# Performance work log

Measured on AMD Instinct MI355X. Metric: run time of the kernel, lower is better.

Reference implementation:

```python
import jax, jax.numpy as jnp
import numpy as np

B, NSL, DS = 8, 12, 768
L, R, DL = 24, 64, 4096
DP = 4096
DIM_T = NSL * 2 * DS          # 18432
FUSED = 1024 + 512            # 1536
GEN_IN = FUSED + 256 + 64     # 1856


def setup_inputs() -> dict:
    key = jax.random.key(0)
    ks = jax.random.split(key, 16)
    s = lambda d: 1.0 / np.sqrt(d)
    return {
        "A_small": jax.random.normal(ks[0], (B, NSL, 1, DS), jnp.float32),
        "B_small": jax.random.normal(ks[1], (B, NSL, DS, 1), jnp.float32),
        "prompt_emb": jax.random.normal(ks[2], (B, DP), jnp.float32),
        "W_ct": jax.random.normal(ks[3], (DIM_T, 1024), jnp.float32) * s(DIM_T),
        "b_ct": jnp.zeros((1024,), jnp.float32),
        "W_cp": jax.random.normal(ks[4], (DP, 512), jnp.float32) * s(DP),
        "b_cp": jnp.zeros((512,), jnp.float32),
        "W_pc": jax.random.normal(ks[5], (FUSED, L), jnp.float32) * s(FUSED),
        "b_pc": jnp.zeros((L,), jnp.float32),
        "E_layer": jax.random.normal(ks[6], (L, 256), jnp.float32),
        "E_chunk": jax.random.normal(ks[7], (R, 64), jnp.float32),
        "W_A": jax.random.normal(ks[8], (GEN_IN, DL), jnp.float32) * s(GEN_IN),
        "b_A": jnp.zeros((DL,), jnp.float32),
        "W_B": jax.random.normal(ks[9], (GEN_IN, DL), jnp.float32) * s(GEN_IN),
        "b_B": jnp.zeros((DL,), jnp.float32),
    }


def reference(A_small, B_small, prompt_emb, W_ct, b_ct, W_cp, b_cp, W_pc, b_pc,
              E_layer, E_chunk, W_A, b_A, W_B, b_B):
    bsz = prompt_emb.shape[0]
    flat_T = jnp.concatenate([A_small.reshape(bsz, -1), B_small.reshape(bsz, -1)], axis=-1)
    t_feat = jax.nn.relu(flat_T @ W_ct + b_ct)          # [B,1024]
    p_feat = jax.nn.relu(prompt_emb @ W_cp + b_cp)      # [B,512]
    fused = jnp.concatenate([t_feat, p_feat], axis=-1)  # [B,1536]
    logits = fused @ W_pc + b_pc                        # [B,L]
    y_soft = jax.nn.sigmoid(logits)                     # eval mode (no gumbel)
    y_hard = (y_soft > 0.5).astype(y_soft.dtype)
    gate = y_soft + jax.lax.stop_gradient(y_hard - y_soft)  # straight-through

    # Batched hypernetwork over all (layer, chunk) pairs instead of a double loop.
    ctx = jnp.broadcast_to(fused[:, None, None, :], (bsz, L, R, FUSED))
    le = jnp.broadcast_to(E_layer[None, :, None, :], (bsz, L, R, 256))
    ce = jnp.broadcast_to(E_chunk[None, None, :, :], (bsz, L, R, 64))
    gen = jnp.concatenate([ctx, le, ce], axis=-1)       # [B,L,R,1856]

    A = gen @ W_A + b_A                                 # [B,L,R,DL]
    Bm = gen @ W_B + b_B                                # [B,L,R,DL]
    A_large = A * gate[:, :, None, None]                # [B,L,R,DL]
    B_large = jnp.transpose(Bm, (0, 1, 3, 2))           # [B,L,DL,R]
    return (A_large, B_large, gate)
```

## Files before the change

kernel.cpp:

```cpp
#include <hip/hip_runtime.h>

typedef float v4f __attribute__((ext_vector_type(4)));

#define NB 8
#define NL 24
#define NR 64
#define ND 4096
#define NFUSED 1536
#define NTF 1024
#define NPF 512
#define KP 4096

#define FKC 12

#define WS_FACC  0
#define WS_GATE  49152
#define WS_PLA   49344
#define WS_PLB   245952
#define WS_CA    442560
#define WS_CBT   704704
#define WS_PFA   966848
#define WS_PFB   1360064

__global__ __launch_bounds__(256) void k_indep(
    const float* __restrict__ As, const float* __restrict__ Bs,
    const float* __restrict__ W_ct,
    const float* __restrict__ prompt, const float* __restrict__ W_cp,
    const float* __restrict__ E_layer, const float* __restrict__ E_chunk,
    const float* __restrict__ W_A, const float* __restrict__ W_B,
    float* __restrict__ fAcc,
    float* __restrict__ pLA, float* __restrict__ pLB,
    float* __restrict__ CA, float* __restrict__ CBT) {
  __shared__ float e[NR * 64];
  const int bx = blockIdx.x;
  const int tid = threadIdx.x;

  if (bx < 576) {
    const int j = (bx & 3) * 256 + tid;
    const int kc = bx >> 2;
    const int kbase = kc * 128;
    float acc[NB] = {};
    for (int kk = 0; kk < 128; ++kk) {
      const int k = kbase + kk;
      const float w = W_ct[(size_t)k * NTF + j];
      const float* x = (k < 9216) ? (As + k) : (Bs + (k - 9216));
#pragma unroll
      for (int b = 0; b < NB; ++b) acc[b] = fmaf(x[b * 9216], w, acc[b]);
    }
    const int rep = kc & 3;
#pragma unroll
    for (int b = 0; b < NB; ++b)
      atomicAdd(fAcc + (size_t)(rep * NB + b) * NFUSED + j, acc[b]);
  } else if (bx < 640) {
    const int t = bx - 576;
    const int j = (t & 1) * 256 + tid;
    const int kc = t >> 1;
    const int kbase = kc * 128;
    float acc[NB] = {};
    for (int kk = 0; kk < 128; ++kk) {
      const int k = kbase + kk;
      const float w = W_cp[(size_t)k * NPF + j];
#pragma unroll
      for (int b = 0; b < NB; ++b) acc[b] = fmaf(prompt[b * KP + k], w, acc[b]);
    }
    const int rep = kc & 3;
#pragma unroll
    for (int b = 0; b < NB; ++b)
      atomicAdd(fAcc + (size_t)(rep * NB + b) * NFUSED + NTF + j, acc[b]);
  } else if (bx < 704) {
    const int t = bx - 640;
    const bool isA = t < 32;
    const int tt = isA ? t : t - 32;
    const int dc = tt & 15;
    const int kh = tt >> 4;
    const float* W = (isA ? W_A : W_B) + (size_t)(NFUSED + kh * 128) * ND;
    float* pL = (isA ? pLA : pLB) + (size_t)kh * NL * ND;
    const int d = dc * 256 + tid;
    float acc[NL] = {};
    for (int kk = 0; kk < 128; ++kk) {
      const float w = W[(size_t)kk * ND + d];
      const float* el = E_layer + kh * 128 + kk;
#pragma unroll
      for (int l = 0; l < NL; ++l) acc[l] = fmaf(el[l * 256], w, acc[l]);
    }
#pragma unroll
    for (int l = 0; l < NL; ++l) pL[(size_t)l * ND + d] = acc[l];
  } else {
    const int t = bx - 704;
    const bool isA = t < 16;
    const int tt = isA ? t : t - 16;
    const float* W = (isA ? W_A : W_B) + (size_t)(NFUSED + 256) * ND;
    for (int i = tid; i < NR * 64; i += 256) e[i] = E_chunk[i];
    __syncthreads();
    const int d = tt * 256 + tid;
    float w[64];
#pragma unroll
    for (int k = 0; k < 64; ++k) w[k] = W[(size_t)k * ND + d];
    for (int r = 0; r < NR; ++r) {
      float s = 0.f;
#pragma unroll
      for (int k = 0; k < 64; ++k) s = fmaf(e[r * 64 + k], w[k], s);
      if (isA) CA[(size_t)r * ND + d] = s;
      else     CBT[(size_t)d * NR + r] = s;
    }
  }
}

__global__ __launch_bounds__(256) void k_dep(
    const float* __restrict__ fAcc,
    const float* __restrict__ b_ct, const float* __restrict__ b_cp,
    const float* __restrict__ W_A, const float* __restrict__ W_B,
    const float* __restrict__ W_pc, const float* __restrict__ b_pc,
    float* __restrict__ pFA, float* __restrict__ pFB,
    float* __restrict__ gate_ws, float* __restrict__ gate_out) {
  __shared__ float sm[1664];
  const int bx = blockIdx.x;
  const int tid = threadIdx.x;

  if (bx < 384) {
    const bool isA = bx < 192;
    const int t = isA ? bx : bx - 192;
    const float* W = isA ? W_A : W_B;
    float* part = isA ? pFA : pFB;
    const int dc = t & 15;
    const int kc = t >> 4;
    const int kbase = kc * 128;

    for (int i = tid; i < 1024; i += 256) {
      const int b = i >> 7, kk = i & 127;
      const int k = kbase + kk;
      float v = (k < NTF) ? b_ct[k] : b_cp[k - NTF];
#pragma unroll
      for (int rep = 0; rep < 4; ++rep)
        v += fAcc[(size_t)(rep * NB + b) * NFUSED + k];
      sm[i] = fmaxf(v, 0.f);
    }
    __syncthreads();

    const int d = dc * 256 + tid;
    float acc[NB] = {};
    for (int kk = 0; kk < 128; ++kk) {
      const float w = W[(size_t)(kbase + kk) * ND + d];
#pragma unroll
      for (int b = 0; b < NB; ++b) acc[b] = fmaf(sm[b * 128 + kk], w, acc[b]);
    }
#pragma unroll
    for (int b = 0; b < NB; ++b)
      part[(size_t)(kc * NB + b) * ND + d] = acc[b];
  } else {
    const int b = bx - 384;
    for (int j = tid; j < NFUSED; j += 256) {
      float v = (j < NTF) ? b_ct[j] : b_cp[j - NTF];
#pragma unroll
      for (int rep = 0; rep < 4; ++rep)
        v += fAcc[(size_t)(rep * NB + b) * NFUSED + j];
      sm[j] = fmaxf(v, 0.f);
    }
    __syncthreads();
    float acc[NL] = {};
    for (int j = tid; j < NFUSED; j += 256) {
      const float f = sm[j];
#pragma unroll
      for (int l = 0; l < NL; ++l) acc[l] = fmaf(f, W_pc[j * NL + l], acc[l]);
    }
#pragma unroll
    for (int off = 32; off > 0; off >>= 1)
#pragma unroll
      for (int l = 0; l < NL; ++l) acc[l] += __shfl_down(acc[l], off);
    const int wave = tid >> 6, lane = tid & 63;
    if (lane == 0)
#pragma unroll
      for (int l = 0; l < NL; ++l) sm[NFUSED + wave * NL + l] = acc[l];
    __syncthreads();
    if (tid < NL) {
      float s = b_pc[tid];
#pragma unroll
      for (int w = 0; w < 4; ++w) s += sm[NFUSED + w * NL + tid];
      const float g = s > 0.f ? 1.f : 0.f;
      gate_ws[b * NL + tid] = g;
      gate_out[b * NL + tid] = g;
    }
  }
}

__global__ __launch_bounds__(256) void k_out(
    const float* __restrict__ pFA, const float* __restrict__ pFB,
    const float* __restrict__ b_A, const float* __restrict__ b_B,
    const float* __restrict__ pLA, const float* __restrict__ pLB,
    const float* __restrict__ CA, const float* __restrict__ CBT,
    const float* __restrict__ gate,
    float* __restrict__ outA, float* __restrict__ outB) {
  __shared__ float sbase[512];
  const int bx = blockIdx.x;
  const int tid = threadIdx.x;
  if (bx < 1536) {
    const int bl = bx >> 3;
    const int rest = bx & 7;
    const int b = bl / NL, l = bl % NL;
    const int d = (rest >> 1) * 1024 + tid * 4;
    const int r0 = (rest & 1) * 32;
    const float g = gate[bl];
    v4f base = *(const v4f*)(b_A + d);
#pragma unroll
    for (int kc = 0; kc < FKC; ++kc)
      base += *(const v4f*)(pFA + (size_t)(kc * NB + b) * ND + d);
    base += *(const v4f*)(pLA + (size_t)l * ND + d);
    base += *(const v4f*)(pLA + (size_t)(NL + l) * ND + d);
    float* outp = outA + ((size_t)bl * NR + r0) * ND + d;
#pragma unroll 4
    for (int r = 0; r < 32; ++r) {
      const v4f c = *(const v4f*)(CA + (size_t)(r0 + r) * ND + d);
      const v4f v = (base + c) * g;
      __builtin_nontemporal_store(v, (v4f*)outp);
      outp += ND;
    }
  } else {
    const int t = bx - 1536;
    const int bl = t >> 3;
    const int b = bl / NL, l = bl % NL;
    const int dbase = (t & 7) * 512;
    for (int dd = tid; dd < 512; dd += 256) {
      const int d = dbase + dd;
      float s = b_B[d] + pLB[(size_t)l * ND + d] + pLB[(size_t)(NL + l) * ND + d];
#pragma unroll
      for (int kc = 0; kc < FKC; ++kc)
        s += pFB[(size_t)(kc * NB + b) * ND + d];
      sbase[dd] = s;
    }
    __syncthreads();
    const int dd16 = tid >> 4;
    const int r4 = (tid & 15) * 4;
#pragma unroll 4
    for (int i = 0; i < 32; ++i) {
      const int dloc = i * 16 + dd16;
      const int d = dbase + dloc;
      const v4f c = *(const v4f*)(CBT + (size_t)d * NR + r4);
      const v4f v = c + sbase[dloc];
      __builtin_nontemporal_store(v, (v4f*)(outB + ((size_t)bl * ND + d) * NR + r4));
    }
  }
}

extern "C" void kernel_launch(void* const* d_in, const int* in_sizes, int n_in,
                              void* d_out, int out_size, void* d_ws, size_t ws_size,
                              hipStream_t stream) {
  const float* A_small   = (const float*)d_in[0];
  const float* B_small   = (const float*)d_in[1];
  const float* prompt    = (const float*)d_in[2];
  const float* W_ct      = (const float*)d_in[3];
  const float* b_ct      = (const float*)d_in[4];
  const float* W_cp      = (const float*)d_in[5];
  const float* b_cp      = (const float*)d_in[6];
  const float* W_pc      = (const float*)d_in[7];
  const float* b_pc      = (const float*)d_in[8];
  const float* E_layer   = (const float*)d_in[9];
  const float* E_chunk   = (const float*)d_in[10];
  const float* W_A       = (const float*)d_in[11];
  const float* b_A       = (const float*)d_in[12];
  const float* W_B       = (const float*)d_in[13];
  const float* b_B       = (const float*)d_in[14];

  float* ws    = (float*)d_ws;
  float* fAcc  = ws + WS_FACC;
  float* gatew = ws + WS_GATE;
  float* pLA   = ws + WS_PLA;
  float* pLB   = ws + WS_PLB;
  float* CA    = ws + WS_CA;
  float* CBT   = ws + WS_CBT;
  float* pFA   = ws + WS_PFA;
  float* pFB   = ws + WS_PFB;

  float* outA = (float*)d_out;
  float* outB = outA + (size_t)192 * NR * ND;
  float* outG = outB + (size_t)192 * ND * NR;

  hipMemsetAsync(fAcc, 0, (size_t)4 * NB * NFUSED * sizeof(float), stream);

  k_indep<<<736, 256, 0, stream>>>(A_small, B_small, W_ct, prompt, W_cp,
                                   E_layer, E_chunk, W_A, W_B,
                                   fAcc, pLA, pLB, CA, CBT);
  k_dep<<<392, 256, 0, stream>>>(fAcc, b_ct, b_cp, W_A, W_B,
                                 W_pc, b_pc, pFA, pFB, gatew, outG);
  k_out<<<3072, 256, 0, stream>>>(pFA, pFB, b_A, b_B, pLA, pLB, CA, CBT,
                                  gatew, outA, outB);
}
```

Measured before the change: 142.8 us.

## Vectorize weight-streaming GEMVs with smaller K chunks and atomic partial reduction

```diff
diff --git a/kernel.cpp b/kernel.cpp
--- a/kernel.cpp
+++ b/kernel.cpp
@@ -11,16 +11,15 @@
 #define NPF 512
 #define KP 4096
 
-#define FKC 12
-
 #define WS_FACC  0
-#define WS_GATE  49152
-#define WS_PLA   49344
-#define WS_PLB   245952
-#define WS_CA    442560
-#define WS_CBT   704704
-#define WS_PFA   966848
-#define WS_PFB   1360064
+#define WS_FAA   98304
+#define WS_FBA   229376
+#define WS_GATE  360448
+#define WS_PLA   360640
+#define WS_PLB   557248
+#define WS_CA    753856
+#define WS_CBT   1016000
+#define WS_ZERO_N 360448
 
 __global__ __launch_bounds__(256) void k_indep(
     const float* __restrict__ As, const float* __restrict__ Bs,
@@ -31,26 +30,34 @@
     float* __restrict__ fAcc,
     float* __restrict__ pLA, float* __restrict__ pLB,
     float* __restrict__ CA, float* __restrict__ CBT) {
-  __shared__ float e[NR * 64];
+  __shared__ float sm[4096];
   const int bx = blockIdx.x;
   const int tid = threadIdx.x;
 
   if (bx < 576) {
-    const int j = (bx & 3) * 256 + tid;
-    const int kc = bx >> 2;
-    const int kbase = kc * 128;
-    float acc[NB] = {};
-    for (int kk = 0; kk < 128; ++kk) {
+    const int kc = bx;
+    const int kbase = kc * 32;
+    if (tid < 256) {
+      const int b = tid >> 5, kk = tid & 31;
       const int k = kbase + kk;
-      const float w = W_ct[(size_t)k * NTF + j];
-      const float* x = (k < 9216) ? (As + k) : (Bs + (k - 9216));
-#pragma unroll
-      for (int b = 0; b < NB; ++b) acc[b] = fmaf(x[b * 9216], w, acc[b]);
-    }
-    const int rep = kc & 3;
-#pragma unroll
-    for (int b = 0; b < NB; ++b)
-      atomicAdd(fAcc + (size_t)(rep * NB + b) * NFUSED + j, acc[b]);
+      sm[tid] = (k < 9216) ? As[b * 9216 + k] : Bs[b * 9216 + (k - 9216)];
+    }
+    __syncthreads();
+    const int j4 = tid * 4;
+    v4f acc[NB] = {};
+#pragma unroll 8
+    for (int kk = 0; kk < 32; ++kk) {
+      const v4f w = *(const v4f*)(W_ct + (size_t)(kbase + kk) * NTF + j4);
+#pragma unroll
+      for (int b = 0; b < NB; ++b) acc[b] += sm[b * 32 + kk] * w;
+    }
+    const int rep = kc & 7;
+#pragma unroll
+    for (int b = 0; b < NB; ++b) {
+      float* dst = fAcc + (size_t)(rep * NB + b) * NFUSED + j4;
+#pragma unroll
+      for (int jj = 0; jj < 4; ++jj) atomicAdd(dst + jj, acc[b][jj]);
+    }
   } else if (bx < 640) {
     const int t = bx - 576;
     const int j = (t & 1) * 256 + tid;
@@ -63,7 +70,7 @@
 #pragma unroll
       for (int b = 0; b < NB; ++b) acc[b] = fmaf(prompt[b * KP + k], w, acc[b]);
     }
-    const int rep = kc & 3;
+    const int rep = kc & 7;
 #pragma unroll
     for (int b = 0; b < NB; ++b)
       atomicAdd(fAcc + (size_t)(rep * NB + b) * NFUSED + NTF + j, acc[b]);
@@ -90,7 +97,7 @@
     const bool isA = t < 16;
     const int tt = isA ? t : t - 16;
     const float* W = (isA ? W_A : W_B) + (size_t)(NFUSED + 256) * ND;
-    for (int i = tid; i < NR * 64; i += 256) e[i] = E_chunk[i];
+    for (int i = tid; i < NR * 64; i += 256) sm[i] = E_chunk[i];
     __syncthreads();
     const int d = tt * 256 + tid;
     float w[64];
@@ -99,7 +106,7 @@
     for (int r = 0; r < NR; ++r) {
       float s = 0.f;
 #pragma unroll
-      for (int k = 0; k < 64; ++k) s = fmaf(e[r * 64 + k], w[k], s);
+      for (int k = 0; k < 64; ++k) s = fmaf(sm[r * 64 + k], w[k], s);
       if (isA) CA[(size_t)r * ND + d] = s;
       else     CBT[(size_t)d * NR + r] = s;
     }
@@ -111,48 +118,53 @@
     const float* __restrict__ b_ct, const float* __restrict__ b_cp,
     const float* __restrict__ W_A, const float* __restrict__ W_B,
     const float* __restrict__ W_pc, const float* __restrict__ b_pc,
-    float* __restrict__ pFA, float* __restrict__ pFB,
+    float* __restrict__ FAa, float* __restrict__ FBa,
     float* __restrict__ gate_ws, float* __restrict__ gate_out) {
   __shared__ float sm[1664];
   const int bx = blockIdx.x;
   const int tid = threadIdx.x;
 
   if (bx < 384) {
-    const bool isA = bx < 192;
-    const int t = isA ? bx : bx - 192;
-    const float* W = isA ? W_A : W_B;
-    float* part = isA ? pFA : pFB;
-    const int dc = t & 15;
-    const int kc = t >> 4;
-    const int kbase = kc * 128;
-
-    for (int i = tid; i < 1024; i += 256) {
-      const int b = i >> 7, kk = i & 127;
+    const bool isB = bx >= 192;
+    const int tt = isB ? bx - 192 : bx;
+    const float* W = isB ? W_B : W_A;
+    float* Fa = isB ? FBa : FAa;
+    const int dc4 = tt & 3;
+    const int kc = tt >> 2;
+    const int kbase = kc * 32;
+
+    if (tid < 256) {
+      const int b = tid >> 5, kk = tid & 31;
       const int k = kbase + kk;
       float v = (k < NTF) ? b_ct[k] : b_cp[k - NTF];
 #pragma unroll
-      for (int rep = 0; rep < 4; ++rep)
+      for (int rep = 0; rep < 8; ++rep)
         v += fAcc[(size_t)(rep * NB + b) * NFUSED + k];
-      sm[i] = fmaxf(v, 0.f);
-    }
-    __syncthreads();
-
-    const int d = dc * 256 + tid;
-    float acc[NB] = {};
-    for (int kk = 0; kk < 128; ++kk) {
-      const float w = W[(size_t)(kbase + kk) * ND + d];
-#pragma unroll
-      for (int b = 0; b < NB; ++b) acc[b] = fmaf(sm[b * 128 + kk], w, acc[b]);
-    }
-#pragma unroll
-    for (int b = 0; b < NB; ++b)
-      part[(size_t)(kc * NB + b) * ND + d] = acc[b];
+      sm[tid] = fmaxf(v, 0.f);
+    }
+    __syncthreads();
+
+    const int d4 = dc4 * 1024 + tid * 4;
+    v4f acc[NB] = {};
+#pragma unroll 8
+    for (int kk = 0; kk < 32; ++kk) {
+      const v4f w = *(const v4f*)(W + (size_t)(kbase + kk) * ND + d4);
+#pragma unroll
+      for (int b = 0; b < NB; ++b) acc[b] += sm[b * 32 + kk] * w;
+    }
+    const int rep = kc & 3;
+#pragma unroll
+    for (int b = 0; b < NB; ++b) {
+      float* dst = Fa + (size_t)(rep * NB + b) * ND + d4;
+#pragma unroll
+      for (int jj = 0; jj < 4; ++jj) atomicAdd(dst + jj, acc[b][jj]);
+    }
   } else {
     const int b = bx - 384;
     for (int j = tid; j < NFUSED; j += 256) {
       float v = (j < NTF) ? b_ct[j] : b_cp[j - NTF];
 #pragma unroll
-      for (int rep = 0; rep < 4; ++rep)
+      for (int rep = 0; rep < 8; ++rep)
         v += fAcc[(size_t)(rep * NB + b) * NFUSED + j];
       sm[j] = fmaxf(v, 0.f);
     }
@@ -184,7 +196,7 @@
 }
 
 __global__ __launch_bounds__(256) void k_out(
-    const float* __restrict__ pFA, const float* __restrict__ pFB,
+    const float* __restrict__ FAa, const float* __restrict__ FBa,
     const float* __restrict__ b_A, const float* __restrict__ b_B,
     const float* __restrict__ pLA, const float* __restrict__ pLB,
     const float* __restrict__ CA, const float* __restrict__ CBT,
@@ -202,8 +214,8 @@
     const float g = gate[bl];
     v4f base = *(const v4f*)(b_A + d);
 #pragma unroll
-    for (int kc = 0; kc < FKC; ++kc)
-      base += *(const v4f*)(pFA + (size_t)(kc * NB + b) * ND + d);
+    for (int rep = 0; rep < 4; ++rep)
+      base += *(const v4f*)(FAa + (size_t)(rep * NB + b) * ND + d);
     base += *(const v4f*)(pLA + (size_t)l * ND + d);
     base += *(const v4f*)(pLA + (size_t)(NL + l) * ND + d);
     float* outp = outA + ((size_t)bl * NR + r0) * ND + d;
@@ -223,8 +235,8 @@
       const int d = dbase + dd;
       float s = b_B[d] + pLB[(size_t)l * ND + d] + pLB[(size_t)(NL + l) * ND + d];
 #pragma unroll
-      for (int kc = 0; kc < FKC; ++kc)
-        s += pFB[(size_t)(kc * NB + b) * ND + d];
+      for (int rep = 0; rep < 4; ++rep)
+        s += FBa[(size_t)(rep * NB + b) * ND + d];
       sbase[dd] = s;
     }
     __syncthreads();
@@ -262,25 +274,25 @@
 
   float* ws    = (float*)d_ws;
   float* fAcc  = ws + WS_FACC;
+  float* FAa   = ws + WS_FAA;
+  float* FBa   = ws + WS_FBA;
   float* gatew = ws + WS_GATE;
   float* pLA   = ws + WS_PLA;
   float* pLB   = ws + WS_PLB;
   float* CA    = ws + WS_CA;
   float* CBT   = ws + WS_CBT;
-  float* pFA   = ws + WS_PFA;
-  float* pFB   = ws + WS_PFB;
 
   float* outA = (float*)d_out;
   float* outB = outA + (size_t)192 * NR * ND;
   float* outG = outB + (size_t)192 * ND * NR;
 
-  hipMemsetAsync(fAcc, 0, (size_t)4 * NB * NFUSED * sizeof(float), stream);
+  hipMemsetAsync(ws, 0, (size_t)WS_ZERO_N * sizeof(float), stream);
 
   k_indep<<<736, 256, 0, stream>>>(A_small, B_small, W_ct, prompt, W_cp,
                                    E_layer, E_chunk, W_A, W_B,
                                    fAcc, pLA, pLB, CA, CBT);
   k_dep<<<392, 256, 0, stream>>>(fAcc, b_ct, b_cp, W_A, W_B,
-                                 W_pc, b_pc, pFA, pFB, gatew, outG);
-  k_out<<<3072, 256, 0, stream>>>(pFA, pFB, b_A, b_B, pLA, pLB, CA, CBT,
+                                 W_pc, b_pc, FAa, FBa, gatew, outG);
+  k_out<<<3072, 256, 0, stream>>>(FAa, FBa, b_A, b_B, pLA, pLB, CA, CBT,
                                   gatew, outA, outB);
 }
```

Result: slower. 239.3 us (+67.6%).

## Reduce fused-context partials via atomics into 4 replicas; restructure A-output blocks

Applied to the files above, without the earlier changes.

```diff
diff --git a/kernel.cpp b/kernel.cpp
--- a/kernel.cpp
+++ b/kernel.cpp
@@ -11,16 +11,15 @@
 #define NPF 512
 #define KP 4096
 
-#define FKC 12
-
 #define WS_FACC  0
-#define WS_GATE  49152
-#define WS_PLA   49344
-#define WS_PLB   245952
-#define WS_CA    442560
-#define WS_CBT   704704
-#define WS_PFA   966848
-#define WS_PFB   1360064
+#define WS_FAA   49152
+#define WS_FBA   180224
+#define WS_GATE  311296
+#define WS_PLA   311488
+#define WS_PLB   508096
+#define WS_CA    704704
+#define WS_CBT   966848
+#define WS_ZERO_N 311296
 
 __global__ __launch_bounds__(256) void k_indep(
     const float* __restrict__ As, const float* __restrict__ Bs,
@@ -111,7 +110,7 @@
     const float* __restrict__ b_ct, const float* __restrict__ b_cp,
     const float* __restrict__ W_A, const float* __restrict__ W_B,
     const float* __restrict__ W_pc, const float* __restrict__ b_pc,
-    float* __restrict__ pFA, float* __restrict__ pFB,
+    float* __restrict__ FAa, float* __restrict__ FBa,
     float* __restrict__ gate_ws, float* __restrict__ gate_out) {
   __shared__ float sm[1664];
   const int bx = blockIdx.x;
@@ -121,7 +120,7 @@
     const bool isA = bx < 192;
     const int t = isA ? bx : bx - 192;
     const float* W = isA ? W_A : W_B;
-    float* part = isA ? pFA : pFB;
+    float* Fa = isA ? FAa : FBa;
     const int dc = t & 15;
     const int kc = t >> 4;
     const int kbase = kc * 128;
@@ -144,9 +143,10 @@
 #pragma unroll
       for (int b = 0; b < NB; ++b) acc[b] = fmaf(sm[b * 128 + kk], w, acc[b]);
     }
+    const int rep = kc & 3;
 #pragma unroll
     for (int b = 0; b < NB; ++b)
-      part[(size_t)(kc * NB + b) * ND + d] = acc[b];
+      atomicAdd(Fa + (size_t)(rep * NB + b) * ND + d, acc[b]);
   } else {
     const int b = bx - 384;
     for (int j = tid; j < NFUSED; j += 256) {
@@ -184,7 +184,7 @@
 }
 
 __global__ __launch_bounds__(256) void k_out(
-    const float* __restrict__ pFA, const float* __restrict__ pFB,
+    const float* __restrict__ FAa, const float* __restrict__ FBa,
     const float* __restrict__ b_A, const float* __restrict__ b_B,
     const float* __restrict__ pLA, const float* __restrict__ pLB,
     const float* __restrict__ CA, const float* __restrict__ CBT,
@@ -195,24 +195,33 @@
   const int tid = threadIdx.x;
   if (bx < 1536) {
     const int bl = bx >> 3;
-    const int rest = bx & 7;
+    const int rg = bx & 7;
     const int b = bl / NL, l = bl % NL;
-    const int d = (rest >> 1) * 1024 + tid * 4;
-    const int r0 = (rest & 1) * 32;
     const float g = gate[bl];
-    v4f base = *(const v4f*)(b_A + d);
-#pragma unroll
-    for (int kc = 0; kc < FKC; ++kc)
-      base += *(const v4f*)(pFA + (size_t)(kc * NB + b) * ND + d);
-    base += *(const v4f*)(pLA + (size_t)l * ND + d);
-    base += *(const v4f*)(pLA + (size_t)(NL + l) * ND + d);
-    float* outp = outA + ((size_t)bl * NR + r0) * ND + d;
-#pragma unroll 4
-    for (int r = 0; r < 32; ++r) {
-      const v4f c = *(const v4f*)(CA + (size_t)(r0 + r) * ND + d);
-      const v4f v = (base + c) * g;
-      __builtin_nontemporal_store(v, (v4f*)outp);
-      outp += ND;
+    const int dt = tid * 4;
+    v4f base[4];
+#pragma unroll
+    for (int seg = 0; seg < 4; ++seg) {
+      const int d = seg * 1024 + dt;
+      v4f v = *(const v4f*)(b_A + d);
+#pragma unroll
+      for (int rep = 0; rep < 4; ++rep)
+        v += *(const v4f*)(FAa + (size_t)(rep * NB + b) * ND + d);
+      v += *(const v4f*)(pLA + (size_t)l * ND + d);
+      v += *(const v4f*)(pLA + (size_t)(NL + l) * ND + d);
+      base[seg] = v;
+    }
+    const int r0 = rg * 8;
+    float* outp = outA + ((size_t)bl * NR + r0) * ND;
+#pragma unroll 2
+    for (int r = 0; r < 8; ++r) {
+#pragma unroll
+      for (int seg = 0; seg < 4; ++seg) {
+        const int d = seg * 1024 + dt;
+        const v4f c = *(const v4f*)(CA + (size_t)(r0 + r) * ND + d);
+        const v4f v = (base[seg] + c) * g;
+        __builtin_nontemporal_store(v, (v4f*)(outp + (size_t)r * ND + d));
+      }
     }
   } else {
     const int t = bx - 1536;
@@ -223,8 +232,8 @@
       const int d = dbase + dd;
       float s = b_B[d] + pLB[(size_t)l * ND + d] + pLB[(size_t)(NL + l) * ND + d];
 #pragma unroll
-      for (int kc = 0; kc < FKC; ++kc)
-        s += pFB[(size_t)(kc * NB + b) * ND + d];
+      for (int rep = 0; rep < 4; ++rep)
+        s += FBa[(size_t)(rep * NB + b) * ND + d];
       sbase[dd] = s;
     }
     __syncthreads();
@@ -262,25 +271,25 @@
 
   float* ws    = (float*)d_ws;
   float* fAcc  = ws + WS_FACC;
+  float* FAa   = ws + WS_FAA;
+  float* FBa   = ws + WS_FBA;
   float* gatew = ws + WS_GATE;
   float* pLA   = ws + WS_PLA;
   float* pLB   = ws + WS_PLB;
   float* CA    = ws + WS_CA;
   float* CBT   = ws + WS_CBT;
-  float* pFA   = ws + WS_PFA;
-  float* pFB   = ws + WS_PFB;
 
   float* outA = (float*)d_out;
   float* outB = outA + (size_t)192 * NR * ND;
   float* outG = outB + (size_t)192 * ND * NR;
 
-  hipMemsetAsync(fAcc, 0, (size_t)4 * NB * NFUSED * sizeof(float), stream);
+  hipMemsetAsync(ws, 0, (size_t)WS_ZERO_N * sizeof(float), stream);
 
   k_indep<<<736, 256, 0, stream>>>(A_small, B_small, W_ct, prompt, W_cp,
                                    E_layer, E_chunk, W_A, W_B,
                                    fAcc, pLA, pLB, CA, CBT);
   k_dep<<<392, 256, 0, stream>>>(fAcc, b_ct, b_cp, W_A, W_B,
-                                 W_pc, b_pc, pFA, pFB, gatew, outG);
-  k_out<<<3072, 256, 0, stream>>>(pFA, pFB, b_A, b_B, pLA, pLB, CA, CBT,
+                                 W_pc, b_pc, FAa, FBa, gatew, outG);
+  k_out<<<3072, 256, 0, stream>>>(FAa, FBa, b_A, b_B, pLA, pLB, CA, CBT,
                                   gatew, outA, outB);
 }
```

Result: no change. 145.4 us (+1.8%).
